# Kernel tuning notes

Hardware: AMD Instinct MI355X
Metric: run time of the kernel (lower is better)

## Reference

```python
import jax, jax.numpy as jnp
import numpy as np

N_NODES = 100000
N_EDGES = 1600000
D_IN = 256
D_OUT = 128


def setup_inputs() -> dict:
    key = jax.random.key(0)
    ks = jax.random.split(key, 7)
    h = jax.random.normal(ks[0], (N_NODES, D_IN), dtype=jnp.float32)
    src = jax.random.randint(ks[1], (N_EDGES,), 0, N_NODES, dtype=jnp.int32)
    dst = jax.random.randint(ks[2], (N_EDGES,), 0, N_NODES, dtype=jnp.int32)
    W = jax.random.normal(ks[3], (D_IN, D_OUT), dtype=jnp.float32) * (1.0 / np.sqrt(D_IN))
    b = jax.random.normal(ks[4], (D_OUT,), dtype=jnp.float32) * 0.01
    w_att = jax.random.normal(ks[5], (2 * D_OUT, 1), dtype=jnp.float32) * (1.0 / np.sqrt(2 * D_OUT))
    b_att = jax.random.normal(ks[6], (1,), dtype=jnp.float32) * 0.01
    return {"h": h, "src": src, "dst": dst, "W": W, "b": b, "w_att": w_att, "b_att": b_att}


def reference(h, src, dst, W, b, w_att, b_att):
    # node projection: graph.ndata['h'] = self.linear(h)
    hp = h @ W + b  # [N, D_OUT]
    n = hp.shape[0]
    d = hp.shape[1]
    # edge attention: leaky_relu(att_linear(cat[h_src, h_dst]))
    # cat([hs, hd]) @ w_att == hs @ w_att[:d] + hd @ w_att[d:]  (avoids [E, 2d] concat)
    wa_s = w_att[:d, 0]  # [D_OUT]
    wa_d = w_att[d:, 0]  # [D_OUT]
    e = hp[src] @ wa_s + hp[dst] @ wa_d + b_att[0]  # [E]
    e = jax.nn.leaky_relu(e)  # default negative_slope 0.01 matches F.leaky_relu
    # segment softmax over each destination node's incoming edges
    emax = jax.ops.segment_max(e, dst, num_segments=n)  # [N]
    ex = jnp.exp(e - emax[dst])  # [E]
    denom = jax.ops.segment_sum(ex, dst, num_segments=n)  # [N]
    # weighted scatter-sum of src features: sum_e alpha_e * h_src_e
    num = jax.ops.segment_sum(ex[:, None] * hp[src], dst, num_segments=n)  # [N, D_OUT]
    out = num / jnp.where(denom > 0, denom, 1.0)[:, None]  # zero-in-degree nodes -> 0
    return out
```

## Files before the change

kernel.cpp:

```cpp
#include <hip/hip_runtime.h>
#include <hip/hip_bf16.h>

#define D_IN 256
#define D_OUT 128
#define BM 128
#define BNODES 64
#define BCAP 1536
#define EPB 8192
#define MAXNB 1600

typedef __attribute__((ext_vector_type(8))) short bf16x8;
typedef __attribute__((ext_vector_type(4))) float f32x4;

__device__ __forceinline__ unsigned short f2bf(float f) {
    unsigned u = __float_as_uint(f);
    unsigned r = ((u >> 16) & 1u) + 0x7FFFu;
    return (unsigned short)((u + r) >> 16);
}
__device__ __forceinline__ unsigned pk2(float a, float b) {
    return (unsigned)f2bf(a) | ((unsigned)f2bf(b) << 16);
}

__global__ __launch_bounds__(256) void init_bcursor_kernel(int* __restrict__ bcursor, int nb)
{
    int i = blockIdx.x * 256 + threadIdx.x;
    if (i < nb) bcursor[i] = i * BCAP;
}

__global__ __launch_bounds__(256) void prep_kernel(
    const float* __restrict__ W, unsigned short* __restrict__ WbT)
{
    int idx = blockIdx.x * 256 + threadIdx.x;
    int k = idx >> 7;
    int c = idx & 127;
    WbT[(size_t)c * 256 + k] = f2bf(W[idx]);
}

__global__ __launch_bounds__(256) void gemm_mfma_kernel(
    const float* __restrict__ h, const unsigned short* __restrict__ WbT,
    const float* __restrict__ b, const float* __restrict__ w_att,
    unsigned short* __restrict__ hpb,
    float* __restrict__ alpha_s, float* __restrict__ alpha_d, int n)
{
    __shared__ char lds[32768];
    __shared__ float als[2][BM], ald[2][BM];
    char* aT = lds;
    char* bT = lds + 16384;

    const int t    = threadIdx.x;
    const int row0 = blockIdx.x * BM;
    const int wv = t >> 6, lane = t & 63;
    const int wr = wv >> 1, wc = wv & 1;
    const int fr = lane & 15, fq = lane >> 4;

    f32x4 acc[4][4];
    #pragma unroll
    for (int m = 0; m < 4; ++m)
        #pragma unroll
        for (int nn = 0; nn < 4; ++nn) acc[m][nn] = (f32x4){0.f, 0.f, 0.f, 0.f};

    const int sr = t >> 1;
    const int sk = (t & 1) * 32;
    const size_t arow = (size_t)((row0 + sr < n) ? (row0 + sr) : (n - 1));
    const float*          asrc = h   + arow * D_IN + sk;
    const unsigned short* bsrc = WbT + (size_t)sr * D_IN + sk;
    const int   wbase = sr * 128 + sk * 2;
    const int   swz   = (sr & 7) << 4;

    for (int kb = 0; kb < 4; ++kb) {
        const float4* as = (const float4*)(asrc + kb * 64);
        #pragma unroll
        for (int c = 0; c < 4; ++c) {
            float4 v0 = as[2 * c], v1 = as[2 * c + 1];
            uint4 p;
            p.x = pk2(v0.x, v0.y); p.y = pk2(v0.z, v0.w);
            p.z = pk2(v1.x, v1.y); p.w = pk2(v1.z, v1.w);
            *(uint4*)(aT + ((wbase + c * 16) ^ swz)) = p;
        }
        const uint4* bs = (const uint4*)(bsrc + kb * 64);
        #pragma unroll
        for (int c = 0; c < 4; ++c)
            *(uint4*)(bT + ((wbase + c * 16) ^ swz)) = bs[c];
        __syncthreads();

        #pragma unroll
        for (int ks = 0; ks < 2; ++ks) {
            bf16x8 af[4], bfr[4];
            #pragma unroll
            for (int m = 0; m < 4; ++m) {
                int row = wr * 64 + m * 16 + fr;
                int o = row * 128 + ks * 64 + fq * 16;
                af[m] = *(const bf16x8*)(aT + (o ^ ((row & 7) << 4)));
            }
            #pragma unroll
            for (int nn = 0; nn < 4; ++nn) {
                int col = wc * 64 + nn * 16 + fr;
                int o = col * 128 + ks * 64 + fq * 16;
                bfr[nn] = *(const bf16x8*)(bT + (o ^ ((col & 7) << 4)));
            }
            #pragma unroll
            for (int m = 0; m < 4; ++m)
                #pragma unroll
                for (int nn = 0; nn < 4; ++nn)
                    acc[m][nn] = __builtin_amdgcn_mfma_f32_16x16x32_bf16(
                        af[m], bfr[nn], acc[m][nn], 0, 0, 0);
        }
        __syncthreads();
    }

    float bcol[4], was[4], wad[4];
    #pragma unroll
    for (int nn = 0; nn < 4; ++nn) {
        int j = wc * 64 + nn * 16 + fr;
        bcol[nn] = b[j];
        was[nn]  = w_att[j];
        wad[nn]  = w_att[D_OUT + j];
    }
    #pragma unroll
    for (int m = 0; m < 4; ++m) {
        #pragma unroll
        for (int reg = 0; reg < 4; ++reg) {
            const int lrow = wr * 64 + m * 16 + fq * 4 + reg;
            const int grow = row0 + lrow;
            float ps = 0.f, pd = 0.f;
            #pragma unroll
            for (int nn = 0; nn < 4; ++nn) {
                float vv = acc[m][nn][reg] + bcol[nn];
                ps += vv * was[nn];
                pd += vv * wad[nn];
                if (grow < n)
                    hpb[(size_t)grow * D_OUT + wc * 64 + nn * 16 + fr] = f2bf(vv);
            }
            #pragma unroll
            for (int o = 1; o < 16; o <<= 1) {
                ps += __shfl_xor(ps, o);
                pd += __shfl_xor(pd, o);
            }
            if (fr == 0) { als[wc][lrow] = ps; ald[wc][lrow] = pd; }
        }
    }
    __syncthreads();
    if (t < BM) {
        int grow = row0 + t;
        if (grow < n) {
            alpha_s[grow] = als[0][t] + als[1][t];
            alpha_d[grow] = ald[0][t] + ald[1][t];
        }
    }
}

__global__ __launch_bounds__(1024) void bucket_scatter_kernel(
    const int* __restrict__ src, const int* __restrict__ dst,
    const float* __restrict__ alpha_s, const float* __restrict__ alpha_d,
    const float* __restrict__ b_att, int* __restrict__ bcursor,
    int2* __restrict__ ebuf, int ne, int nb)
{
    __shared__ int lhist[MAXNB];
    __shared__ int gbase[MAXNB];
    __shared__ int lcur[MAXNB];
    const int t = threadIdx.x;
    for (int i = t; i < nb; i += 1024) { lhist[i] = 0; lcur[i] = 0; }
    __syncthreads();
    const int base = blockIdx.x * EPB;
    #pragma unroll
    for (int j = 0; j < EPB / 1024; ++j) {
        int idx = base + j * 1024 + t;
        if (idx < ne) atomicAdd(&lhist[dst[idx] >> 6], 1);
    }
    __syncthreads();
    for (int i = t; i < nb; i += 1024) {
        int c = lhist[i];
        gbase[i] = c ? atomicAdd(&bcursor[i], c) : 0;
    }
    __syncthreads();
    const float ba = b_att[0];
    #pragma unroll
    for (int j = 0; j < EPB / 1024; ++j) {
        int idx = base + j * 1024 + t;
        if (idx < ne) {
            int s = src[idx], d = dst[idx];
            float ev = alpha_s[s] + alpha_d[d] + ba;
            ev = (ev >= 0.f) ? ev : 0.01f * ev;
            int bkt = d >> 6;
            int pos = gbase[bkt] + atomicAdd(&lcur[bkt], 1);
            if (pos < (bkt + 1) * BCAP)
                ebuf[pos] = make_int2(s | ((d & 63) << 17), __float_as_int(ev));
        }
    }
}

#define ACCUM8(uvar, wvar)                                     \
    acc[0] += (wvar) * __uint_as_float((uvar).x << 16);        \
    acc[1] += (wvar) * __uint_as_float((uvar).x & 0xFFFF0000u);\
    acc[2] += (wvar) * __uint_as_float((uvar).y << 16);        \
    acc[3] += (wvar) * __uint_as_float((uvar).y & 0xFFFF0000u);\
    acc[4] += (wvar) * __uint_as_float((uvar).z << 16);        \
    acc[5] += (wvar) * __uint_as_float((uvar).z & 0xFFFF0000u);\
    acc[6] += (wvar) * __uint_as_float((uvar).w << 16);        \
    acc[7] += (wvar) * __uint_as_float((uvar).w & 0xFFFF0000u);

__global__ __launch_bounds__(512) void aggregate_kernel(
    const unsigned short* __restrict__ hpb, const int2* __restrict__ ebuf,
    const int* __restrict__ bcursor, float* __restrict__ out, int n)
{
    __shared__ int2 srec[BCAP];
    __shared__ int lhist[BNODES], lstart[BNODES], lcur[BNODES];
    const int t = threadIdx.x;
    const int bk = blockIdx.x;
    const int node0 = bk << 6;
    const int base = bk * BCAP;
    int cnt = bcursor[bk] - base;
    cnt = min(cnt, BCAP);

    if (t < BNODES) lhist[t] = 0;
    __syncthreads();
    for (int i = t; i < cnt; i += 512)
        atomicAdd(&lhist[(ebuf[base + i].x >> 17) & 63], 1);
    __syncthreads();
    if (t < BNODES) {
        int c0 = lhist[t];
        int incl = c0;
        #pragma unroll
        for (int o = 1; o < 64; o <<= 1) {
            int v = __shfl_up(incl, o);
            if (t >= o) incl += v;
        }
        lstart[t] = incl - c0;
        lcur[t]   = incl - c0;
    }
    __syncthreads();
    for (int i = t; i < cnt; i += 512) {
        int2 r = ebuf[base + i];
        int pos = atomicAdd(&lcur[(r.x >> 17) & 63], 1);
        srec[pos] = r;
    }
    __syncthreads();

    const int wv = t >> 6, lane = t & 63;
    const int q = lane >> 4, dlane = lane & 15;
    const uint4* hp4 = (const uint4*)hpb;

    #pragma unroll
    for (int p = 0; p < 2; ++p) {
        const int nd = p * 32 + wv * 4 + q;
        const int gnode = node0 + nd;
        const int off = lstart[nd], c = lhist[nd];

        float m = -INFINITY;
        for (int i = dlane; i < c; i += 16)
            m = fmaxf(m, __int_as_float(srec[off + i].y));
        #pragma unroll
        for (int o = 8; o; o >>= 1) m = fmaxf(m, __shfl_xor(m, o));

        float acc[8] = {0.f,0.f,0.f,0.f,0.f,0.f,0.f,0.f};
        float denom = 0.f;

        #pragma unroll 2
        for (int t0 = 0; t0 < c; ++t0) {
            int2 r = srec[off + t0];
            float w = __expf(__int_as_float(r.y) - m);
            int s = r.x & 0x1FFFF;
            uint4 u = hp4[(size_t)s * 16 + dlane];
            ACCUM8(u, w)
            denom += w;
        }

        if (gnode < n) {
            float inv = (c > 0) ? 1.f / denom : 0.f;
            float4 o0 = { acc[0]*inv, acc[1]*inv, acc[2]*inv, acc[3]*inv };
            float4 o1 = { acc[4]*inv, acc[5]*inv, acc[6]*inv, acc[7]*inv };
            float4* op = (float4*)(out + (size_t)gnode * D_OUT) + 2 * dlane;
            op[0] = o0;
            op[1] = o1;
        }
    }
}

extern "C" void kernel_launch(void* const* d_in, const int* in_sizes, int n_in,
                              void* d_out, int out_size, void* d_ws, size_t ws_size,
                              hipStream_t stream)
{
    const float* h     = (const float*)d_in[0];
    const int*   src   = (const int*)  d_in[1];
    const int*   dst   = (const int*)  d_in[2];
    const float* W     = (const float*)d_in[3];
    const float* b     = (const float*)d_in[4];
    const float* w_att = (const float*)d_in[5];
    const float* b_att = (const float*)d_in[6];
    float* out = (float*)d_out;

    const int n  = in_sizes[0] / D_IN;
    const int ne = in_sizes[1];
    const int nb = (n + BNODES - 1) / BNODES;

    unsigned short* hpb = (unsigned short*)d_ws;
    float* alpha_s = (float*)d_ws + (size_t)n * 64;
    float* alpha_d = alpha_s + n;
    int2*  ebuf    = (int2*)(alpha_d + n);
    int*   bcursor = (int*)(ebuf + (size_t)nb * BCAP);
    unsigned short* WbT = (unsigned short*)(bcursor + nb);

    init_bcursor_kernel<<<(nb + 255) / 256, 256, 0, stream>>>(bcursor, nb);
    prep_kernel<<<128, 256, 0, stream>>>(W, WbT);
    gemm_mfma_kernel<<<(n + BM - 1) / BM, 256, 0, stream>>>(
        h, WbT, b, w_att, hpb, alpha_s, alpha_d, n);
    bucket_scatter_kernel<<<(ne + EPB - 1) / EPB, 1024, 0, stream>>>(
        src, dst, alpha_s, alpha_d, b_att, bcursor, ebuf, ne, nb);
    aggregate_kernel<<<nb, 512, 0, stream>>>(hpb, ebuf, bcursor, out, n);
}
```

Before: 151.8 us.

## Restructure projection GEMM to keep full W in LDS and unroll gather loop

The GEMM now loads all of the bf16 transposed W (64KB) into LDS once through direct global-to-LDS loads. Each wave then owns 64 rows across all 128 output columns, streaming its A rows from global memory straight into registers with double buffering. This removes the A staging through LDS, the per-k-block barriers and the cross-wave alpha reduction. The aggregate loop is unrolled by four with clamped indices so more independent gathers are in flight. In exchange, the GEMM uses more LDS and registers per block, has fewer blocks, and its A global loads are not coalesced.

```diff
diff --git a/kernel.cpp b/kernel.cpp
--- a/kernel.cpp
+++ b/kernel.cpp
@@ -3,7 +3,6 @@
 
 #define D_IN 256
 #define D_OUT 128
-#define BM 128
 #define BNODES 64
 #define BCAP 1536
 #define EPB 8192
@@ -20,6 +19,17 @@
 __device__ __forceinline__ unsigned pk2(float a, float b) {
     return (unsigned)f2bf(a) | ((unsigned)f2bf(b) << 16);
 }
+__device__ __forceinline__ bf16x8 pack8(float4 a, float4 b) {
+    union { uint4 u; bf16x8 v; } r;
+    r.u.x = pk2(a.x, a.y); r.u.y = pk2(a.z, a.w);
+    r.u.z = pk2(b.x, b.y); r.u.w = pk2(b.z, b.w);
+    return r.v;
+}
+__device__ __forceinline__ void gload_lds16(const void* g, void* l) {
+    __builtin_amdgcn_global_load_lds(
+        (const __attribute__((address_space(1))) void*)g,
+        (__attribute__((address_space(3))) void*)l, 16, 0, 0);
+}
 
 __global__ __launch_bounds__(256) void init_bcursor_kernel(int* __restrict__ bcursor, int nb)
 {
@@ -36,115 +46,104 @@
     WbT[(size_t)c * 256 + k] = f2bf(W[idx]);
 }
 
-__global__ __launch_bounds__(256) void gemm_mfma_kernel(
+__global__ __launch_bounds__(256, 2) void gemm_mfma_kernel(
     const float* __restrict__ h, const unsigned short* __restrict__ WbT,
     const float* __restrict__ b, const float* __restrict__ w_att,
     unsigned short* __restrict__ hpb,
     float* __restrict__ alpha_s, float* __restrict__ alpha_d, int n)
 {
-    __shared__ char lds[32768];
-    __shared__ float als[2][BM], ald[2][BM];
-    char* aT = lds;
-    char* bT = lds + 16384;
-
-    const int t    = threadIdx.x;
-    const int row0 = blockIdx.x * BM;
+    __shared__ char bT[65536];
+    const int t = threadIdx.x;
     const int wv = t >> 6, lane = t & 63;
-    const int wr = wv >> 1, wc = wv & 1;
     const int fr = lane & 15, fq = lane >> 4;
-
-    f32x4 acc[4][4];
+    const int r0 = blockIdx.x * 256 + wv * 64;
+    const int swz = (fr & 7) << 4;
+
+    {
+        #pragma unroll
+        for (int j = 0; j < 16; ++j) {
+            int col = wv * 32 + j * 2 + (lane >> 5);
+            int seg = lane & 31;
+            const char* src = (const char*)WbT + col * 512 + ((seg * 16) ^ ((col & 7) << 4));
+            char* dst = bT + (wv * 32 + j * 2) * 512;
+            gload_lds16(src, dst);
+        }
+    }
+    __syncthreads();
+
+    const float* arow[4];
+    #pragma unroll
+    for (int m = 0; m < 4; ++m) {
+        int rg = r0 + m * 16 + fr;
+        if (rg >= n) rg = n - 1;
+        arow[m] = h + (size_t)rg * D_IN + fq * 8;
+    }
+
+    f32x4 acc[4][8];
     #pragma unroll
     for (int m = 0; m < 4; ++m)
         #pragma unroll
-        for (int nn = 0; nn < 4; ++nn) acc[m][nn] = (f32x4){0.f, 0.f, 0.f, 0.f};
-
-    const int sr = t >> 1;
-    const int sk = (t & 1) * 32;
-    const size_t arow = (size_t)((row0 + sr < n) ? (row0 + sr) : (n - 1));
-    const float*          asrc = h   + arow * D_IN + sk;
-    const unsigned short* bsrc = WbT + (size_t)sr * D_IN + sk;
-    const int   wbase = sr * 128 + sk * 2;
-    const int   swz   = (sr & 7) << 4;
-
-    for (int kb = 0; kb < 4; ++kb) {
-        const float4* as = (const float4*)(asrc + kb * 64);
-        #pragma unroll
-        for (int c = 0; c < 4; ++c) {
-            float4 v0 = as[2 * c], v1 = as[2 * c + 1];
-            uint4 p;
-            p.x = pk2(v0.x, v0.y); p.y = pk2(v0.z, v0.w);
-            p.z = pk2(v1.x, v1.y); p.w = pk2(v1.z, v1.w);
-            *(uint4*)(aT + ((wbase + c * 16) ^ swz)) = p;
-        }
-        const uint4* bs = (const uint4*)(bsrc + kb * 64);
-        #pragma unroll
-        for (int c = 0; c < 4; ++c)
-            *(uint4*)(bT + ((wbase + c * 16) ^ swz)) = bs[c];
-        __syncthreads();
-
-        #pragma unroll
-        for (int ks = 0; ks < 2; ++ks) {
-            bf16x8 af[4], bfr[4];
+        for (int nn = 0; nn < 8; ++nn) acc[m][nn] = (f32x4){0.f, 0.f, 0.f, 0.f};
+
+    float4 bufA[2][4][2];
+    #pragma unroll
+    for (int m = 0; m < 4; ++m) {
+        const float4* ap = (const float4*)arow[m];
+        bufA[0][m][0] = ap[0]; bufA[0][m][1] = ap[1];
+    }
+
+    #pragma unroll
+    for (int ks = 0; ks < 8; ++ks) {
+        const int cur = ks & 1, nxt = cur ^ 1;
+        if (ks < 7) {
             #pragma unroll
             for (int m = 0; m < 4; ++m) {
-                int row = wr * 64 + m * 16 + fr;
-                int o = row * 128 + ks * 64 + fq * 16;
-                af[m] = *(const bf16x8*)(aT + (o ^ ((row & 7) << 4)));
+                const float4* ap = (const float4*)(arow[m] + (ks + 1) * 32);
+                bufA[nxt][m][0] = ap[0]; bufA[nxt][m][1] = ap[1];
             }
-            #pragma unroll
-            for (int nn = 0; nn < 4; ++nn) {
-                int col = wc * 64 + nn * 16 + fr;
-                int o = col * 128 + ks * 64 + fq * 16;
-                bfr[nn] = *(const bf16x8*)(bT + (o ^ ((col & 7) << 4)));
-            }
+        }
+        bf16x8 af[4];
+        #pragma unroll
+        for (int m = 0; m < 4; ++m)
+            af[m] = pack8(bufA[cur][m][0], bufA[cur][m][1]);
+
+        #pragma unroll
+        for (int nn = 0; nn < 8; ++nn) {
+            bf16x8 bfr = *(const bf16x8*)(bT + nn * 8192 + fr * 512
+                            + ((ks * 64 + fq * 16) ^ swz));
             #pragma unroll
             for (int m = 0; m < 4; ++m)
-                #pragma unroll
-                for (int nn = 0; nn < 4; ++nn)
-                    acc[m][nn] = __builtin_amdgcn_mfma_f32_16x16x32_bf16(
-                        af[m], bfr[nn], acc[m][nn], 0, 0, 0);
-        }
-        __syncthreads();
-    }
-
-    float bcol[4], was[4], wad[4];
-    #pragma unroll
-    for (int nn = 0; nn < 4; ++nn) {
-        int j = wc * 64 + nn * 16 + fr;
-        bcol[nn] = b[j];
-        was[nn]  = w_att[j];
-        wad[nn]  = w_att[D_OUT + j];
+                acc[m][nn] = __builtin_amdgcn_mfma_f32_16x16x32_bf16(
+                    af[m], bfr, acc[m][nn], 0, 0, 0);
+        }
+    }
+
+    float bcol[8], was[8], wad[8];
+    #pragma unroll
+    for (int nn = 0; nn < 8; ++nn) {
+        int j = nn * 16 + fr;
+        bcol[nn] = b[j]; was[nn] = w_att[j]; wad[nn] = w_att[D_OUT + j];
     }
     #pragma unroll
     for (int m = 0; m < 4; ++m) {
         #pragma unroll
         for (int reg = 0; reg < 4; ++reg) {
-            const int lrow = wr * 64 + m * 16 + fq * 4 + reg;
-            const int grow = row0 + lrow;
+            const int grow = r0 + m * 16 + fq * 4 + reg;
+            const bool ok = grow < n;
             float ps = 0.f, pd = 0.f;
             #pragma unroll
-            for (int nn = 0; nn < 4; ++nn) {
+            for (int nn = 0; nn < 8; ++nn) {
                 float vv = acc[m][nn][reg] + bcol[nn];
                 ps += vv * was[nn];
                 pd += vv * wad[nn];
-                if (grow < n)
-                    hpb[(size_t)grow * D_OUT + wc * 64 + nn * 16 + fr] = f2bf(vv);
+                if (ok) hpb[(size_t)grow * D_OUT + nn * 16 + fr] = f2bf(vv);
             }
             #pragma unroll
             for (int o = 1; o < 16; o <<= 1) {
                 ps += __shfl_xor(ps, o);
                 pd += __shfl_xor(pd, o);
             }
-            if (fr == 0) { als[wc][lrow] = ps; ald[wc][lrow] = pd; }
-        }
-    }
-    __syncthreads();
-    if (t < BM) {
-        int grow = row0 + t;
-        if (grow < n) {
-            alpha_s[grow] = als[0][t] + als[1][t];
-            alpha_d[grow] = ald[0][t] + ald[1][t];
+            if (fr == 0 && ok) { alpha_s[grow] = ps; alpha_d[grow] = pd; }
         }
     }
 }
@@ -255,14 +254,24 @@
         float acc[8] = {0.f,0.f,0.f,0.f,0.f,0.f,0.f,0.f};
         float denom = 0.f;
 
-        #pragma unroll 2
-        for (int t0 = 0; t0 < c; ++t0) {
-            int2 r = srec[off + t0];
-            float w = __expf(__int_as_float(r.y) - m);
-            int s = r.x & 0x1FFFF;
-            uint4 u = hp4[(size_t)s * 16 + dlane];
-            ACCUM8(u, w)
-            denom += w;
+        for (int t0 = 0; t0 < c; t0 += 4) {
+            const int cm1 = c - 1;
+            int2 r0 = srec[off + min(t0 + 0, cm1)];
+            int2 r1 = srec[off + min(t0 + 1, cm1)];
+            int2 r2 = srec[off + min(t0 + 2, cm1)];
+            int2 r3 = srec[off + min(t0 + 3, cm1)];
+            float w0 = __expf(__int_as_float(r0.y) - m);
+            float w1 = (t0 + 1 < c) ? __expf(__int_as_float(r1.y) - m) : 0.f;
+            float w2 = (t0 + 2 < c) ? __expf(__int_as_float(r2.y) - m) : 0.f;
+            float w3 = (t0 + 3 < c) ? __expf(__int_as_float(r3.y) - m) : 0.f;
+            uint4 u0 = hp4[(size_t)(r0.x & 0x1FFFF) * 16 + dlane];
+            uint4 u1 = hp4[(size_t)(r1.x & 0x1FFFF) * 16 + dlane];
+            uint4 u2 = hp4[(size_t)(r2.x & 0x1FFFF) * 16 + dlane];
+            uint4 u3 = hp4[(size_t)(r3.x & 0x1FFFF) * 16 + dlane];
+            ACCUM8(u0, w0) denom += w0;
+            ACCUM8(u1, w1) denom += w1;
+            ACCUM8(u2, w2) denom += w2;
+            ACCUM8(u3, w3) denom += w3;
         }
 
         if (gnode < n) {
@@ -302,7 +311,7 @@
 
     init_bcursor_kernel<<<(nb + 255) / 256, 256, 0, stream>>>(bcursor, nb);
     prep_kernel<<<128, 256, 0, stream>>>(W, WbT);
-    gemm_mfma_kernel<<<(n + BM - 1) / BM, 256, 0, stream>>>(
+    gemm_mfma_kernel<<<(n + 255) / 256, 256, 0, stream>>>(
         h, WbT, b, w_att, hpb, alpha_s, alpha_d, n);
     bucket_scatter_kernel<<<(ne + EPB - 1) / EPB, 1024, 0, stream>>>(
         src, dst, alpha_s, alpha_d, b_att, bcursor, ebuf, ne, nb);
```

Measured after the change: 137.3 us. 1.11x faster.
